# Performance work log

Measured on AMD Instinct MI355X. Metric: run time of the kernel, lower is better.

The kernel has to match this reference:

```python
import jax, jax.numpy as jnp
import numpy as np

N, D = 8192, 128
WEIGHT = 0.01


def _neg_flat_indices(n):
    # Replicates: mask = ones(n,n); fill_diagonal_(0); mask[i,i+1]=0; mask[i+1,i]=0
    # i.e. keep (i,j) with j != i, j != i+1, j != i-1. Row-major flatnonzero
    # reproduces torch's sim[mask] flattening order exactly.
    i = np.arange(n)[:, None]
    j = np.arange(n)[None, :]
    mask = (j != i) & (j != i + 1) & (j != i - 1)
    idx = np.flatnonzero(mask)
    assert idx.size == (n - 1) * (n - 2)
    return idx


NEG_IDX = jnp.asarray(_neg_flat_indices(N))  # [(N-1)*(N-2)] int32/int64 constant


def setup_inputs() -> dict:
    key = jax.random.key(0)
    factor = jax.random.normal(key, (N, D), dtype=jnp.float32)
    return {"factor": factor}


def reference(factor):
    n = factor.shape[0]
    # F.normalize(factor): L2-normalize rows with eps=1e-12
    norms = jnp.linalg.norm(factor, axis=1, keepdims=True)
    f = factor / jnp.maximum(norms, 1e-12)
    sim = f @ f.T                                   # [N, N] gram matrix
    pos = jnp.diagonal(sim, offset=1).reshape(n - 1, 1)      # [N-1, 1]
    neg = sim.reshape(-1)[NEG_IDX].reshape(n - 1, n - 2)     # [N-1, N-2]
    logits = jnp.concatenate([pos, neg], axis=1)             # [N-1, N-1]
    # CrossEntropyLoss(reduction='sum') with all-zero labels:
    # sum_i (logsumexp(logits_i) - logits_i[0])
    loss = jnp.sum(jax.nn.logsumexp(logits, axis=1) - logits[:, 0])
    loss = loss / n
    return -WEIGHT * loss
```

## Files before the change

### kernel.cpp

```cpp
#include <hip/hip_runtime.h>
#include <hip/hip_bf16.h>

#define N 8192
#define D 128
#define WEIGHT 0.01f
#define NTILES 64
#define NBLK 2080

typedef __bf16 bf16x8 __attribute__((ext_vector_type(8)));
typedef float floatx4 __attribute__((ext_vector_type(4)));

__global__ __launch_bounds__(256) void k_norm(const float* __restrict__ x,
                                              __hip_bfloat16* __restrict__ fb) {
    int gid = blockIdx.x * 256 + threadIdx.x;
    int row = gid >> 6;
    int lane = gid & 63;
    const float* xr = x + row * D;
    float a0 = xr[lane];
    float a1 = xr[lane + 64];
    float s = a0 * a0 + a1 * a1;
    #pragma unroll
    for (int m = 1; m < 64; m <<= 1) s += __shfl_xor(s, m, 64);
    float inv = 1.0f / fmaxf(sqrtf(s), 1e-12f);
    fb[row * D + lane]      = __float2bfloat16(a0 * inv);
    fb[row * D + lane + 64] = __float2bfloat16(a1 * inv);
}

__global__ __launch_bounds__(512, 4) void k_gram(const __hip_bfloat16* __restrict__ fb,
                                                 float* __restrict__ Prow,
                                                 float* __restrict__ Pcol,
                                                 float* __restrict__ p,
                                                 float* __restrict__ ep) {
    int b = blockIdx.x;
    int bi = (int)((2.0 * NTILES + 1.0 - sqrt((2.0 * NTILES + 1.0) * (2.0 * NTILES + 1.0) - 8.0 * (double)b)) * 0.5);
    while (bi * NTILES - bi * (bi - 1) / 2 > b) --bi;
    while ((bi + 1) * NTILES - (bi + 1) * bi / 2 <= b) ++bi;
    int bj = bi + (b - (bi * NTILES - bi * (bi - 1) / 2));

    __shared__ uint4 Ab[128 * 16];
    __shared__ uint4 Bb[128 * 16];
    __shared__ float PR[4][128];
    __shared__ float PC[2][128];
    const int t = threadIdx.x;
    const int rbase = bi * 128, cbase = bj * 128;
    const uint4* g = (const uint4*)fb;
    #pragma unroll
    for (int k = 0; k < 4; ++k) {
        int idx = t + k * 512;
        int row = idx >> 4, c16 = idx & 15;
        int sw = c16 ^ (row & 15);
        Ab[row * 16 + sw] = g[(rbase + row) * 16 + c16];
        Bb[row * 16 + sw] = g[(cbase + row) * 16 + c16];
    }
    __syncthreads();

    const int lane = t & 63;
    const int wid  = t >> 6;
    const int wrow = wid >> 2, wcol = wid & 3;
    const int col0 = lane & 15;
    const int quad = lane >> 4;

    floatx4 acc[4][2];
    #pragma unroll
    for (int a = 0; a < 4; ++a)
        #pragma unroll
        for (int c = 0; c < 2; ++c)
            acc[a][c] = (floatx4){0.0f, 0.0f, 0.0f, 0.0f};

    #pragma unroll
    for (int ks = 0; ks < 4; ++ks) {
        bf16x8 af[4], bfr[2];
        int j = ks * 4 + quad;
        int jsw = j ^ col0;
        #pragma unroll
        for (int mt = 0; mt < 4; ++mt) {
            int rl = wrow * 64 + mt * 16 + col0;
            af[mt] = *(const bf16x8*)&Ab[rl * 16 + jsw];
        }
        #pragma unroll
        for (int nt = 0; nt < 2; ++nt) {
            int cl = wcol * 32 + nt * 16 + col0;
            bfr[nt] = *(const bf16x8*)&Bb[cl * 16 + jsw];
        }
        #pragma unroll
        for (int mt = 0; mt < 4; ++mt)
            #pragma unroll
            for (int nt = 0; nt < 2; ++nt)
                acc[mt][nt] = __builtin_amdgcn_mfma_f32_16x16x32_bf16(af[mt], bfr[nt], acc[mt][nt], 0, 0, 0);
    }

    float rowpart[4][4];
    float colpart[2];
    #pragma unroll
    for (int a = 0; a < 4; ++a)
        #pragma unroll
        for (int c = 0; c < 4; ++c) rowpart[a][c] = 0.0f;
    colpart[0] = colpart[1] = 0.0f;

    if (bj > bi + 1) {
        #pragma unroll
        for (int mt = 0; mt < 4; ++mt)
            #pragma unroll
            for (int nt = 0; nt < 2; ++nt)
                #pragma unroll
                for (int reg = 0; reg < 4; ++reg) {
                    float e = __expf(acc[mt][nt][reg]);
                    rowpart[mt][reg] += e;
                    colpart[nt] += e;
                }
    } else {
        #pragma unroll
        for (int mt = 0; mt < 4; ++mt)
            #pragma unroll
            for (int nt = 0; nt < 2; ++nt)
                #pragma unroll
                for (int reg = 0; reg < 4; ++reg) {
                    int r = rbase + wrow * 64 + mt * 16 + quad * 4 + reg;
                    int c = cbase + wcol * 32 + nt * 16 + col0;
                    float v = acc[mt][nt][reg];
                    float e = __expf(v);
                    if (c == r + 1) { p[r] = v; ep[r] = e; }
                    e = (c > r) ? e : 0.0f;
                    rowpart[mt][reg] += e;
                    colpart[nt] += e;
                }
    }

    #pragma unroll
    for (int mt = 0; mt < 4; ++mt) {
        #pragma unroll
        for (int reg = 0; reg < 4; ++reg) {
            float v = rowpart[mt][reg];
            v += __shfl_xor(v, 1, 64);
            v += __shfl_xor(v, 2, 64);
            v += __shfl_xor(v, 4, 64);
            v += __shfl_xor(v, 8, 64);
            if (col0 == 0)
                PR[wcol][wrow * 64 + mt * 16 + quad * 4 + reg] = v;
        }
    }
    #pragma unroll
    for (int nt = 0; nt < 2; ++nt) {
        float v = colpart[nt];
        v += __shfl_xor(v, 16, 64);
        v += __shfl_xor(v, 32, 64);
        if (quad == 0)
            PC[wrow][wcol * 32 + nt * 16 + col0] = v;
    }
    __syncthreads();

    if (t < 128) {
        Prow[(size_t)b * 128 + t] = PR[0][t] + PR[1][t] + PR[2][t] + PR[3][t];
    } else if (t < 256) {
        int c = t - 128;
        Pcol[(size_t)b * 128 + c] = PC[0][c] + PC[1][c];
    }
}

__global__ __launch_bounds__(256) void k_reduce(const float* __restrict__ Prow,
                                                const float* __restrict__ Pcol,
                                                float* __restrict__ U,
                                                float* __restrict__ L) {
    int tile = blockIdx.x;
    int tid = threadIdx.x;
    int base_t = tile * NTILES - tile * (tile - 1) / 2;
    if (tid < 128) {
        float s = 0.0f;
        for (int bj = tile; bj < NTILES; ++bj)
            s += Prow[(size_t)(base_t + bj - tile) * 128 + tid];
        U[tile * 128 + tid] = s;
    } else {
        int c = tid - 128;
        float s = 0.0f;
        for (int bi = 0; bi <= tile; ++bi) {
            int bb = bi * NTILES - bi * (bi - 1) / 2 + (tile - bi);
            s += Pcol[(size_t)bb * 128 + c];
        }
        L[tile * 128 + c] = s;
    }
}

__global__ __launch_bounds__(1024) void k_final(const float* __restrict__ U,
                                                const float* __restrict__ L,
                                                const float* __restrict__ p,
                                                const float* __restrict__ ep,
                                                float* __restrict__ out) {
    __shared__ float swred[16];
    float s = 0.0f;
    for (int i = threadIdx.x; i < N - 1; i += 1024) {
        float tt = U[i] + L[i + 1] - ep[i];
        s += __logf(tt) - p[i];
    }
    #pragma unroll
    for (int m = 1; m < 64; m <<= 1) s += __shfl_xor(s, m, 64);
    int lane = threadIdx.x & 63, wid = threadIdx.x >> 6;
    if (lane == 0) swred[wid] = s;
    __syncthreads();
    if (threadIdx.x == 0) {
        float tot = 0.0f;
        #pragma unroll
        for (int w = 0; w < 16; ++w) tot += swred[w];
        out[0] = -WEIGHT * tot / (float)N;
    }
}

extern "C" void kernel_launch(void* const* d_in, const int* in_sizes, int n_in,
                              void* d_out, int out_size, void* d_ws, size_t ws_size,
                              hipStream_t stream) {
    const float* x = (const float*)d_in[0];
    float* out = (float*)d_out;
    char* ws = (char*)d_ws;
    __hip_bfloat16* fb = (__hip_bfloat16*)ws;
    float* p    = (float*)(ws + (size_t)N * D * 2);
    float* ep   = p + N;
    float* U    = ep + N;
    float* L    = U + N;
    float* Prow = L + N;
    float* Pcol = Prow + (size_t)NBLK * 128;

    hipLaunchKernelGGL(k_norm,   dim3(2048), dim3(256),  0, stream, x, fb);
    hipLaunchKernelGGL(k_gram,   dim3(NBLK), dim3(512),  0, stream, fb, Prow, Pcol, p, ep);
    hipLaunchKernelGGL(k_reduce, dim3(64),   dim3(256),  0, stream, Prow, Pcol, U, L);
    hipLaunchKernelGGL(k_final,  dim3(1),    dim3(1024), 0, stream, U, L, p, ep, out);
}
```

Measured before the change: 107.1 us.

## Load MFMA fragments directly from global and use transpose-butterfly reductions

Removes the shared-memory staging of the A/B tiles, so each lane now loads its bf16x8 MFMA fragments straight from global memory, relying on L2/L1 since the 2 MB normalized matrix is reused heavily. The row and column partial-sum reductions switch from independent xor-shuffle trees per value to a transposing butterfly that halves the live values at each step, cutting the shuffle count. Launch bounds rise to 6 blocks per CU, since the LDS footprint is much smaller now. The trade-off is uncoalesced, strided global fragment loads and more dependence on the caches.

```diff
diff --git a/kernel.cpp b/kernel.cpp
--- a/kernel.cpp
+++ b/kernel.cpp
@@ -26,7 +26,7 @@
     fb[row * D + lane + 64] = __float2bfloat16(a1 * inv);
 }
 
-__global__ __launch_bounds__(512, 4) void k_gram(const __hip_bfloat16* __restrict__ fb,
+__global__ __launch_bounds__(512, 6) void k_gram(const __hip_bfloat16* __restrict__ fb,
                                                  float* __restrict__ Prow,
                                                  float* __restrict__ Pcol,
                                                  float* __restrict__ p,
@@ -37,28 +37,17 @@
     while ((bi + 1) * NTILES - (bi + 1) * bi / 2 <= b) ++bi;
     int bj = bi + (b - (bi * NTILES - bi * (bi - 1) / 2));
 
-    __shared__ uint4 Ab[128 * 16];
-    __shared__ uint4 Bb[128 * 16];
     __shared__ float PR[4][128];
     __shared__ float PC[2][128];
+
     const int t = threadIdx.x;
-    const int rbase = bi * 128, cbase = bj * 128;
-    const uint4* g = (const uint4*)fb;
-    #pragma unroll
-    for (int k = 0; k < 4; ++k) {
-        int idx = t + k * 512;
-        int row = idx >> 4, c16 = idx & 15;
-        int sw = c16 ^ (row & 15);
-        Ab[row * 16 + sw] = g[(rbase + row) * 16 + c16];
-        Bb[row * 16 + sw] = g[(cbase + row) * 16 + c16];
-    }
-    __syncthreads();
-
     const int lane = t & 63;
     const int wid  = t >> 6;
     const int wrow = wid >> 2, wcol = wid & 3;
     const int col0 = lane & 15;
     const int quad = lane >> 4;
+    const int rbase = bi * 128, cbase = bj * 128;
+    const uint4* g = (const uint4*)fb;
 
     floatx4 acc[4][2];
     #pragma unroll
@@ -69,18 +58,17 @@
 
     #pragma unroll
     for (int ks = 0; ks < 4; ++ks) {
+        int j = ks * 4 + quad;
         bf16x8 af[4], bfr[2];
-        int j = ks * 4 + quad;
-        int jsw = j ^ col0;
         #pragma unroll
         for (int mt = 0; mt < 4; ++mt) {
-            int rl = wrow * 64 + mt * 16 + col0;
-            af[mt] = *(const bf16x8*)&Ab[rl * 16 + jsw];
+            int r = rbase + wrow * 64 + mt * 16 + col0;
+            af[mt] = *(const bf16x8*)&g[(size_t)r * 16 + j];
         }
         #pragma unroll
         for (int nt = 0; nt < 2; ++nt) {
-            int cl = wcol * 32 + nt * 16 + col0;
-            bfr[nt] = *(const bf16x8*)&Bb[cl * 16 + jsw];
+            int c = cbase + wcol * 32 + nt * 16 + col0;
+            bfr[nt] = *(const bf16x8*)&g[(size_t)c * 16 + j];
         }
         #pragma unroll
         for (int mt = 0; mt < 4; ++mt)
@@ -89,12 +77,10 @@
                 acc[mt][nt] = __builtin_amdgcn_mfma_f32_16x16x32_bf16(af[mt], bfr[nt], acc[mt][nt], 0, 0, 0);
     }
 
-    float rowpart[4][4];
+    float v[16];
     float colpart[2];
     #pragma unroll
-    for (int a = 0; a < 4; ++a)
-        #pragma unroll
-        for (int c = 0; c < 4; ++c) rowpart[a][c] = 0.0f;
+    for (int m = 0; m < 16; ++m) v[m] = 0.0f;
     colpart[0] = colpart[1] = 0.0f;
 
     if (bj > bi + 1) {
@@ -105,7 +91,7 @@
                 #pragma unroll
                 for (int reg = 0; reg < 4; ++reg) {
                     float e = __expf(acc[mt][nt][reg]);
-                    rowpart[mt][reg] += e;
+                    v[mt * 4 + reg] += e;
                     colpart[nt] += e;
                 }
     } else {
@@ -117,35 +103,55 @@
                 for (int reg = 0; reg < 4; ++reg) {
                     int r = rbase + wrow * 64 + mt * 16 + quad * 4 + reg;
                     int c = cbase + wcol * 32 + nt * 16 + col0;
-                    float v = acc[mt][nt][reg];
-                    float e = __expf(v);
-                    if (c == r + 1) { p[r] = v; ep[r] = e; }
+                    float s0 = acc[mt][nt][reg];
+                    float e = __expf(s0);
+                    if (c == r + 1) { p[r] = s0; ep[r] = e; }
                     e = (c > r) ? e : 0.0f;
-                    rowpart[mt][reg] += e;
+                    v[mt * 4 + reg] += e;
                     colpart[nt] += e;
                 }
     }
 
-    #pragma unroll
-    for (int mt = 0; mt < 4; ++mt) {
-        #pragma unroll
-        for (int reg = 0; reg < 4; ++reg) {
-            float v = rowpart[mt][reg];
-            v += __shfl_xor(v, 1, 64);
-            v += __shfl_xor(v, 2, 64);
-            v += __shfl_xor(v, 4, 64);
-            v += __shfl_xor(v, 8, 64);
-            if (col0 == 0)
-                PR[wcol][wrow * 64 + mt * 16 + quad * 4 + reg] = v;
-        }
-    }
-    #pragma unroll
-    for (int nt = 0; nt < 2; ++nt) {
-        float v = colpart[nt];
-        v += __shfl_xor(v, 16, 64);
-        v += __shfl_xor(v, 32, 64);
-        if (quad == 0)
-            PC[wrow][wcol * 32 + nt * 16 + col0] = v;
+    float v8[8];
+    #pragma unroll
+    for (int k = 0; k < 8; ++k) {
+        float a = v[2 * k], bb = v[2 * k + 1];
+        float give = (lane & 1) ? a : bb;
+        float keep = (lane & 1) ? bb : a;
+        v8[k] = keep + __shfl_xor(give, 1, 64);
+    }
+    float v4[4];
+    #pragma unroll
+    for (int k = 0; k < 4; ++k) {
+        float a = v8[2 * k], bb = v8[2 * k + 1];
+        float give = (lane & 2) ? a : bb;
+        float keep = (lane & 2) ? bb : a;
+        v4[k] = keep + __shfl_xor(give, 2, 64);
+    }
+    float v2[2];
+    #pragma unroll
+    for (int k = 0; k < 2; ++k) {
+        float a = v4[2 * k], bb = v4[2 * k + 1];
+        float give = (lane & 4) ? a : bb;
+        float keep = (lane & 4) ? bb : a;
+        v2[k] = keep + __shfl_xor(give, 4, 64);
+    }
+    {
+        float a = v2[0], bb = v2[1];
+        float give = (lane & 8) ? a : bb;
+        float keep = (lane & 8) ? bb : a;
+        float v1 = keep + __shfl_xor(give, 8, 64);
+        int rowl = wrow * 64 + (col0 >> 2) * 16 + quad * 4 + (col0 & 3);
+        PR[wcol][rowl] = v1;
+    }
+
+    {
+        float give = (lane & 16) ? colpart[0] : colpart[1];
+        float keep = (lane & 16) ? colpart[1] : colpart[0];
+        float cv = keep + __shfl_xor(give, 16, 64);
+        cv += __shfl_xor(cv, 32, 64);
+        if (lane < 32)
+            PC[wrow][wcol * 32 + lane] = cv;
     }
     __syncthreads();
 
```

Result: slower. 130.9 us (+22.2%).
